# Kernel optimization log

Measured on AMD Instinct MI355X. Metric: run time of the kernel, lower is better.

## Reference

```python
import jax, jax.numpy as jnp
import numpy as np

G = 8          # grid_size
NUM_HEADS = 8


def setup_inputs() -> dict:
    key = jax.random.key(0)
    ks = jax.random.split(key, 4)
    B, H, W, C = 32, 64, 64, 256
    x = jax.random.normal(ks[0], (B, H, W, C), dtype=jnp.float32)
    w_qkv = jax.random.normal(ks[1], (3 * C, C), dtype=jnp.float32) * (C ** -0.5)
    b_qkv = jnp.zeros((3 * C,), dtype=jnp.float32)
    w_proj = jax.random.normal(ks[2], (C, C), dtype=jnp.float32) * (C ** -0.5)
    b_proj = jnp.zeros((C,), dtype=jnp.float32)
    return {"x": x, "w_qkv": w_qkv, "b_qkv": b_qkv, "w_proj": w_proj, "b_proj": b_proj}


def reference(x, w_qkv, b_qkv, w_proj, b_proj):
    B, H, W, C = x.shape
    g = G
    nh = NUM_HEADS
    hd = C // nh
    scale = hd ** -0.5
    Hp, Wp = H // g, W // g
    # grid partition: [B,H,W,C] -> [B*Hp*Wp, g*g, C]
    t = x.reshape(B, g, Hp, g, Wp, C)
    t = t.transpose(0, 2, 4, 1, 3, 5).reshape(B * Hp * Wp, g * g, C)
    Bg, N = t.shape[0], g * g
    # qkv projection (torch Linear: x @ W.T + b)
    qkv = t @ w_qkv.T + b_qkv                       # [Bg, N, 3C]
    qkv = qkv.reshape(Bg, N, 3, nh, hd).transpose(2, 0, 3, 1, 4)  # [3, Bg, nh, N, hd]
    q, k, v = qkv[0], qkv[1], qkv[2]
    attn = jnp.einsum('bhnd,bhmd->bhnm', q, k) * scale
    attn = jax.nn.softmax(attn, axis=-1)
    out = jnp.einsum('bhnm,bhmd->bhnd', attn, v)    # [Bg, nh, N, hd]
    out = out.transpose(0, 2, 1, 3).reshape(Bg, N, C)
    out = out @ w_proj.T + b_proj
    # grid unpartition: [Bg, g, g, C] -> [B, H, W, C]
    out = out.reshape(B, Hp, Wp, g, g, C).transpose(0, 3, 1, 4, 2, 5).reshape(B, H, W, C)
    return out
```

## Files before the change

### kernel.cpp

```cpp
#include <hip/hip_runtime.h>

typedef __attribute__((ext_vector_type(8))) short bf16x8;
typedef __attribute__((ext_vector_type(4))) float f32x4;
typedef __attribute__((ext_vector_type(4))) short s16x4;

#define MFMA16(a, b, c) __builtin_amdgcn_mfma_f32_16x16x32_bf16((a), (b), (c), 0, 0, 0)

__device__ __forceinline__ short f2bf(float f) {
    union { float f; unsigned u; } v; v.f = f;
    return (short)((v.u + 0x7FFFu + ((v.u >> 16) & 1u)) >> 16);
}
__device__ __forceinline__ s16x4 cvt4(f32x4 v) {
    s16x4 r; r[0] = f2bf(v[0]); r[1] = f2bf(v[1]); r[2] = f2bf(v[2]); r[3] = f2bf(v[3]); return r;
}
__device__ __forceinline__ f32x4 fzero4() { f32x4 z; z[0]=0.f; z[1]=0.f; z[2]=0.f; z[3]=0.f; return z; }

__global__ __launch_bounds__(256, 1)
void convw_kernel(const float* __restrict__ wqkv, const float* __restrict__ wproj,
                  short* __restrict__ wsb)
{
    int i = (blockIdx.x * 256 + threadIdx.x) * 8;
    const float* src = (i < 196608) ? (wqkv + i) : (wproj + (i - 196608));
    *(s16x4*)(wsb + i)     = cvt4(*(const f32x4*)(src));
    *(s16x4*)(wsb + i + 4) = cvt4(*(const f32x4*)(src + 4));
}

#define SMEM_BYTES 52224


#define QK_ST(HL, MH, B)  { \
    _Pragma("unroll") \
    for (int n2 = 0; n2 < 2; ++n2) { \
      _Pragma("unroll") \
      for (int m2 = 0; m2 < 2; ++m2) { \
        s16x4 pk; \
        _Pragma("unroll") \
        for (int r = 0; r < 4; ++r) \
          pk[r] = f2bf(acc[2*(HL)+n2][2*(MH)+m2][r] + bq[2*(HL)+n2][r]); \
        *(s16x4*)((B) + (m2*16 + l16)*36 + n2*16 + q4*4) = pk; \
      } \
    } }

#define QK_RD(HL, MH, B, DST)  { \
    _Pragma("unroll") \
    for (int m2 = 0; m2 < 2; ++m2) \
      DST[HL][2*(MH)+m2] = *(const bf16x8*)((B) + (m2*16 + l16)*36 + q4*8); }

#define QK_ROUNDS(DST) \
    QK_ST(0,0,SW0) QK_ST(0,1,SW1) QK_RD(0,0,SW0,DST) QK_ST(1,0,SW0) \
    QK_RD(0,1,SW1,DST) QK_ST(1,1,SW1) QK_RD(1,0,SW0,DST) QK_RD(1,1,SW1,DST)

#define P_ST(KT, MH, B)  { \
    _Pragma("unroll") \
    for (int n2 = 0; n2 < 2; ++n2) { \
      _Pragma("unroll") \
      for (int m2 = 0; m2 < 2; ++m2) { \
        s16x4 pk; \
        _Pragma("unroll") \
        for (int r = 0; r < 4; ++r) \
          pk[r] = f2bf(s[2*(KT)+n2][2*(MH)+m2][r]); \
        *(s16x4*)((B) + (m2*16 + l16)*36 + n2*16 + q4*4) = pk; \
      } \
    } }

#define P_RD(MH, B)  { \
    _Pragma("unroll") \
    for (int m2 = 0; m2 < 2; ++m2) \
      pa[2*(MH)+m2] = *(const bf16x8*)((B) + (m2*16 + l16)*36 + q4*8); }

__global__ __launch_bounds__(256, 3)
void ga2d_kernel(const float* __restrict__ x,
                 const short* __restrict__ wsb,
                 const float* __restrict__ bqkv,
                 const float* __restrict__ bproj,
                 float* __restrict__ out)
{
    extern __shared__ short smem[];
    short* XA = smem;
    const int tid  = threadIdx.x;
    const int w    = tid >> 6;
    const int lane = tid & 63;
    const int l16  = lane & 15;
    const int q4   = lane >> 4;
    short* SW0 = smem + 16896 + w * 2304;
    short* SW1 = SW0 + 1152;

    const int blk = blockIdx.x;
    const int bb  = blk >> 6;
    const int hp  = (blk >> 3) & 7;
    const int wp  = blk & 7;
    const size_t gbase = (size_t)bb * 64 * 64 * 256;

    #pragma unroll
    for (int i = 0; i < 16; ++i) {
        int id  = i * 256 + tid;
        int tok = id >> 6, c4 = id & 63;
        int hr  = (tok >> 3) * 8 + hp;
        int wc  = (tok & 7) * 8 + wp;
        f32x4 v = *(const f32x4*)(x + gbase + ((size_t)hr * 64 + wc) * 256 + c4 * 4);
        *(s16x4*)(XA + tok * 264 + c4 * 4) = cvt4(v);
    }
    __syncthreads();

    bf16x8 qa[2][4], kb[2][4], vb[2][2][2];
    #pragma unroll
    for (int g3 = 0; g3 < 2; ++g3) {
        const short* WB = wsb + (size_t)(g3 * 256 + w * 64) * 256;
        f32x4 acc[4][4];
        #pragma unroll
        for (int n = 0; n < 4; ++n)
            #pragma unroll
            for (int m = 0; m < 4; ++m) acc[n][m] = fzero4();
        #pragma unroll
        for (int k = 0; k < 8; ++k) {
            const int koff = k * 32 + q4 * 8;
            bf16x8 a[4], bw[4];
            #pragma unroll
            for (int m = 0; m < 4; ++m)
                a[m] = *(const bf16x8*)(XA + (m * 16 + l16) * 264 + koff);
            #pragma unroll
            for (int n = 0; n < 4; ++n)
                bw[n] = *(const bf16x8*)(WB + (size_t)(n * 16 + l16) * 256 + koff);
            #pragma unroll
            for (int n = 0; n < 4; ++n)
                #pragma unroll
                for (int m = 0; m < 4; ++m)
                    acc[n][m] = MFMA16(bw[n], a[m], acc[n][m]);
        }
        f32x4 bq[4];
        #pragma unroll
        for (int n = 0; n < 4; ++n)
            bq[n] = *(const f32x4*)(bqkv + g3 * 256 + w * 64 + n * 16 + q4 * 4);
        if (g3 == 0) { QK_ROUNDS(qa) } else { QK_ROUNDS(kb) }
    }
    {
        float bv[4];
        #pragma unroll
        for (int n = 0; n < 4; ++n) bv[n] = bqkv[512 + w * 64 + n * 16 + l16];
        #pragma unroll
        for (int vh = 0; vh < 2; ++vh) {
            const short* WB = wsb + (size_t)(512 + w * 64 + vh * 32) * 256;
            f32x4 acc2[2][4];
            #pragma unroll
            for (int n2 = 0; n2 < 2; ++n2)
                #pragma unroll
                for (int m = 0; m < 4; ++m) acc2[n2][m] = fzero4();
            #pragma unroll
            for (int k = 0; k < 8; ++k) {
                const int koff = k * 32 + q4 * 8;
                bf16x8 a[4], bw2[2];
                #pragma unroll
                for (int m = 0; m < 4; ++m)
                    a[m] = *(const bf16x8*)(XA + (m * 16 + l16) * 264 + koff);
                #pragma unroll
                for (int n2 = 0; n2 < 2; ++n2)
                    bw2[n2] = *(const bf16x8*)(WB + (size_t)(n2 * 16 + l16) * 256 + koff);
                #pragma unroll
                for (int n2 = 0; n2 < 2; ++n2)
                    #pragma unroll
                    for (int m = 0; m < 4; ++m)
                        acc2[n2][m] = MFMA16(a[m], bw2[n2], acc2[n2][m]);
            }
            #pragma unroll
            for (int kt = 0; kt < 2; ++kt) {
                short* B = kt ? SW1 : SW0;
                #pragma unroll
                for (int n2 = 0; n2 < 2; ++n2)
                    #pragma unroll
                    for (int m2 = 0; m2 < 2; ++m2) {
                        s16x4 pk;
                        #pragma unroll
                        for (int r = 0; r < 4; ++r)
                            pk[r] = f2bf(acc2[n2][2 * kt + m2][r] + bv[2 * vh + n2]);
                        *(s16x4*)(B + (n2 * 16 + l16) * 36 + m2 * 16 + q4 * 4) = pk;
                    }
            }
            #pragma unroll
            for (int kt = 0; kt < 2; ++kt) {
                const short* B = kt ? SW1 : SW0;
                #pragma unroll
                for (int dt = 0; dt < 2; ++dt)
                    vb[vh][dt][kt] = *(const bf16x8*)(B + (dt * 16 + l16) * 36 + q4 * 8);
            }
        }
    }
    __syncthreads();

    const float kscl = 0.25503546f;
    #pragma unroll
    for (int hl = 0; hl < 2; ++hl) {
        f32x4 s[4][4];
        #pragma unroll
        for (int n = 0; n < 4; ++n)
            #pragma unroll
            for (int m = 0; m < 4; ++m)
                s[n][m] = MFMA16(kb[hl][n], qa[hl][m], fzero4());

        float rinv[4];
        #pragma unroll
        for (int m = 0; m < 4; ++m) {
            float v0 = fmaxf(fmaxf(s[0][m][0], s[0][m][1]), fmaxf(s[0][m][2], s[0][m][3]));
            float v1 = fmaxf(fmaxf(s[1][m][0], s[1][m][1]), fmaxf(s[1][m][2], s[1][m][3]));
            float v2 = fmaxf(fmaxf(s[2][m][0], s[2][m][1]), fmaxf(s[2][m][2], s[2][m][3]));
            float v3 = fmaxf(fmaxf(s[3][m][0], s[3][m][1]), fmaxf(s[3][m][2], s[3][m][3]));
            float v  = fmaxf(fmaxf(v0, v1), fmaxf(v2, v3));
            v = fmaxf(v, __shfl_xor(v, 16));
            v = fmaxf(v, __shfl_xor(v, 32));
            float t = 0.f;
            #pragma unroll
            for (int n = 0; n < 4; ++n)
                #pragma unroll
                for (int r = 0; r < 4; ++r) {
                    float e = exp2f((s[n][m][r] - v) * kscl);
                    s[n][m][r] = e;
                    t += e;
                }
            t += __shfl_xor(t, 16);
            t += __shfl_xor(t, 32);
            rinv[m] = 1.0f / t;
        }

        f32x4 o2[2][4];
        #pragma unroll
        for (int dt = 0; dt < 2; ++dt)
            #pragma unroll
            for (int m = 0; m < 4; ++m) o2[dt][m] = fzero4();
        #pragma unroll
        for (int kt = 0; kt < 2; ++kt) {
            bf16x8 pa[4];
            P_ST(kt,0,SW0) P_ST(kt,1,SW1) P_RD(0,SW0) P_RD(1,SW1)
            #pragma unroll
            for (int m = 0; m < 4; ++m)
                #pragma unroll
                for (int dt = 0; dt < 2; ++dt)
                    o2[dt][m] = MFMA16(vb[hl][dt][kt], pa[m], o2[dt][m]);
        }
        #pragma unroll
        for (int dt = 0; dt < 2; ++dt)
            #pragma unroll
            for (int m = 0; m < 4; ++m) {
                s16x4 pk;
                #pragma unroll
                for (int r = 0; r < 4; ++r) pk[r] = f2bf(o2[dt][m][r] * rinv[m]);
                *(s16x4*)(XA + (m * 16 + l16) * 264 + w * 64 + hl * 32 + dt * 16 + q4 * 4) = pk;
            }
    }
    __syncthreads();

    {
        const short* WPb = wsb + 196608 + (size_t)(w * 64) * 256;
        f32x4 pc[4][4];
        #pragma unroll
        for (int n = 0; n < 4; ++n)
            #pragma unroll
            for (int m = 0; m < 4; ++m) pc[n][m] = fzero4();
        #pragma unroll
        for (int k = 0; k < 8; ++k) {
            const int koff = k * 32 + q4 * 8;
            bf16x8 a[4], bw[4];
            #pragma unroll
            for (int m = 0; m < 4; ++m)
                a[m] = *(const bf16x8*)(XA + (m * 16 + l16) * 264 + koff);
            #pragma unroll
            for (int n = 0; n < 4; ++n)
                bw[n] = *(const bf16x8*)(WPb + (size_t)(n * 16 + l16) * 256 + koff);
            #pragma unroll
            for (int n = 0; n < 4; ++n)
                #pragma unroll
                for (int m = 0; m < 4; ++m)
                    pc[n][m] = MFMA16(a[m], bw[n], pc[n][m]);
        }
        #pragma unroll
        for (int n = 0; n < 4; ++n) {
            const int col  = w * 64 + n * 16 + l16;
            const float bi = bproj[col];
            #pragma unroll
            for (int m = 0; m < 4; ++m) {
                #pragma unroll
                for (int r = 0; r < 4; ++r) {
                    const int tok = m * 16 + q4 * 4 + r;
                    const int hr  = (tok >> 3) * 8 + hp;
                    const int wc  = (tok & 7) * 8 + wp;
                    out[gbase + ((size_t)hr * 64 + wc) * 256 + col] = pc[n][m][r] + bi;
                }
            }
        }
    }
}

extern "C" void kernel_launch(void* const* d_in, const int* in_sizes, int n_in,
                              void* d_out, int out_size, void* d_ws, size_t ws_size,
                              hipStream_t stream) {
    const float* x     = (const float*)d_in[0];
    const float* wqkv  = (const float*)d_in[1];
    const float* bqkv  = (const float*)d_in[2];
    const float* wproj = (const float*)d_in[3];
    const float* bproj = (const float*)d_in[4];
    float*       out   = (float*)d_out;
    short*       wsb   = (short*)d_ws;

    convw_kernel<<<128, 256, 0, stream>>>(wqkv, wproj, wsb);

    hipFuncSetAttribute(reinterpret_cast<const void*>(ga2d_kernel),
                        hipFuncAttributeMaxDynamicSharedMemorySize, SMEM_BYTES);
    ga2d_kernel<<<2048, 256, SMEM_BYTES, stream>>>(x, wsb, bqkv, bproj, out);
}
```

Measured before the change: 366.3 us.

## Use 8 waves per block with one head per wave and drop softmax max

The block grows from 4 to 8 waves, so each wave handles one attention head and a 32-column slice of each projection, cutting per-wave register pressure and raising parallelism. Shared memory grows to hold per-wave scratch for 8 waves. Softmax now skips the row-max subtraction and accumulates exp sums while streaming P to shared memory. That removes a reduction pass, but exp2 of unshifted scores can overflow for larger logits.

```diff
diff --git a/kernel.cpp b/kernel.cpp
--- a/kernel.cpp
+++ b/kernel.cpp
@@ -25,50 +25,44 @@
     *(s16x4*)(wsb + i + 4) = cvt4(*(const f32x4*)(src + 4));
 }
 
-#define SMEM_BYTES 52224
-
-
-#define QK_ST(HL, MH, B)  { \
-    _Pragma("unroll") \
-    for (int n2 = 0; n2 < 2; ++n2) { \
-      _Pragma("unroll") \
-      for (int m2 = 0; m2 < 2; ++m2) { \
-        s16x4 pk; \
-        _Pragma("unroll") \
-        for (int r = 0; r < 4; ++r) \
-          pk[r] = f2bf(acc[2*(HL)+n2][2*(MH)+m2][r] + bq[2*(HL)+n2][r]); \
-        *(s16x4*)((B) + (m2*16 + l16)*36 + n2*16 + q4*4) = pk; \
-      } \
+#define SMEM_BYTES 70656
+
+#define QKGEMM(G3, DST) { \
+    const short* WB = wsb + (size_t)((G3) * 256 + w * 32) * 256; \
+    f32x4 acc[2][4]; \
+    _Pragma("unroll") for (int n2 = 0; n2 < 2; ++n2) \
+      _Pragma("unroll") for (int m = 0; m < 4; ++m) acc[n2][m] = fzero4(); \
+    _Pragma("unroll") for (int k = 0; k < 8; ++k) { \
+        const int koff = k * 32 + q4 * 8; \
+        bf16x8 a[4], bw[2]; \
+        _Pragma("unroll") for (int m = 0; m < 4; ++m) \
+            a[m] = *(const bf16x8*)(XA + (m * 16 + l16) * 264 + koff); \
+        _Pragma("unroll") for (int n2 = 0; n2 < 2; ++n2) \
+            bw[n2] = *(const bf16x8*)(WB + (size_t)(n2 * 16 + l16) * 256 + koff); \
+        _Pragma("unroll") for (int n2 = 0; n2 < 2; ++n2) \
+          _Pragma("unroll") for (int m = 0; m < 4; ++m) \
+            acc[n2][m] = MFMA16(bw[n2], a[m], acc[n2][m]); \
+    } \
+    f32x4 bq[2]; \
+    _Pragma("unroll") for (int n2 = 0; n2 < 2; ++n2) \
+        bq[n2] = *(const f32x4*)(bqkv + (G3) * 256 + w * 32 + n2 * 16 + q4 * 4); \
+    _Pragma("unroll") for (int MH = 0; MH < 2; ++MH) { \
+        short* B = MH ? SW1 : SW0; \
+        _Pragma("unroll") for (int n2 = 0; n2 < 2; ++n2) \
+          _Pragma("unroll") for (int m2 = 0; m2 < 2; ++m2) { \
+            s16x4 pk; \
+            _Pragma("unroll") for (int r = 0; r < 4; ++r) \
+                pk[r] = f2bf(acc[n2][2 * MH + m2][r] + bq[n2][r]); \
+            *(s16x4*)(B + (m2 * 16 + l16) * 36 + n2 * 16 + q4 * 4) = pk; \
+        } \
+    } \
+    _Pragma("unroll") for (int MH = 0; MH < 2; ++MH) { \
+        const short* B = MH ? SW1 : SW0; \
+        _Pragma("unroll") for (int m2 = 0; m2 < 2; ++m2) \
+            DST[2 * MH + m2] = *(const bf16x8*)(B + (m2 * 16 + l16) * 36 + q4 * 8); \
     } }
 
-#define QK_RD(HL, MH, B, DST)  { \
-    _Pragma("unroll") \
-    for (int m2 = 0; m2 < 2; ++m2) \
-      DST[HL][2*(MH)+m2] = *(const bf16x8*)((B) + (m2*16 + l16)*36 + q4*8); }
-
-#define QK_ROUNDS(DST) \
-    QK_ST(0,0,SW0) QK_ST(0,1,SW1) QK_RD(0,0,SW0,DST) QK_ST(1,0,SW0) \
-    QK_RD(0,1,SW1,DST) QK_ST(1,1,SW1) QK_RD(1,0,SW0,DST) QK_RD(1,1,SW1,DST)
-
-#define P_ST(KT, MH, B)  { \
-    _Pragma("unroll") \
-    for (int n2 = 0; n2 < 2; ++n2) { \
-      _Pragma("unroll") \
-      for (int m2 = 0; m2 < 2; ++m2) { \
-        s16x4 pk; \
-        _Pragma("unroll") \
-        for (int r = 0; r < 4; ++r) \
-          pk[r] = f2bf(s[2*(KT)+n2][2*(MH)+m2][r]); \
-        *(s16x4*)((B) + (m2*16 + l16)*36 + n2*16 + q4*4) = pk; \
-      } \
-    } }
-
-#define P_RD(MH, B)  { \
-    _Pragma("unroll") \
-    for (int m2 = 0; m2 < 2; ++m2) \
-      pa[2*(MH)+m2] = *(const bf16x8*)((B) + (m2*16 + l16)*36 + q4*8); }
-
-__global__ __launch_bounds__(256, 3)
+__global__ __launch_bounds__(512, 4)
 void ga2d_kernel(const float* __restrict__ x,
                  const short* __restrict__ wsb,
                  const float* __restrict__ bqkv,
@@ -92,8 +86,8 @@
     const size_t gbase = (size_t)bb * 64 * 64 * 256;
 
     #pragma unroll
-    for (int i = 0; i < 16; ++i) {
-        int id  = i * 256 + tid;
+    for (int i = 0; i < 8; ++i) {
+        int id  = i * 512 + tid;
         int tok = id >> 6, c4 = id & 63;
         int hr  = (tok >> 3) * 8 + hp;
         int wc  = (tok & 7) * 8 + wp;
@@ -102,138 +96,113 @@
     }
     __syncthreads();
 
-    bf16x8 qa[2][4], kb[2][4], vb[2][2][2];
-    #pragma unroll
-    for (int g3 = 0; g3 < 2; ++g3) {
-        const short* WB = wsb + (size_t)(g3 * 256 + w * 64) * 256;
-        f32x4 acc[4][4];
-        #pragma unroll
-        for (int n = 0; n < 4; ++n)
-            #pragma unroll
-            for (int m = 0; m < 4; ++m) acc[n][m] = fzero4();
+    bf16x8 qa[4], kb[4], vb[2][2];
+    {
+        const short* WB = wsb + (size_t)(512 + w * 32) * 256;
+        f32x4 acc[2][4];
+        #pragma unroll
+        for (int n2 = 0; n2 < 2; ++n2)
+            #pragma unroll
+            for (int m = 0; m < 4; ++m) acc[n2][m] = fzero4();
         #pragma unroll
         for (int k = 0; k < 8; ++k) {
             const int koff = k * 32 + q4 * 8;
-            bf16x8 a[4], bw[4];
+            bf16x8 a[4], bw[2];
             #pragma unroll
             for (int m = 0; m < 4; ++m)
                 a[m] = *(const bf16x8*)(XA + (m * 16 + l16) * 264 + koff);
             #pragma unroll
-            for (int n = 0; n < 4; ++n)
-                bw[n] = *(const bf16x8*)(WB + (size_t)(n * 16 + l16) * 256 + koff);
-            #pragma unroll
-            for (int n = 0; n < 4; ++n)
+            for (int n2 = 0; n2 < 2; ++n2)
+                bw[n2] = *(const bf16x8*)(WB + (size_t)(n2 * 16 + l16) * 256 + koff);
+            #pragma unroll
+            for (int n2 = 0; n2 < 2; ++n2)
                 #pragma unroll
                 for (int m = 0; m < 4; ++m)
-                    acc[n][m] = MFMA16(bw[n], a[m], acc[n][m]);
-        }
-        f32x4 bq[4];
-        #pragma unroll
-        for (int n = 0; n < 4; ++n)
-            bq[n] = *(const f32x4*)(bqkv + g3 * 256 + w * 64 + n * 16 + q4 * 4);
-        if (g3 == 0) { QK_ROUNDS(qa) } else { QK_ROUNDS(kb) }
-    }
+                    acc[n2][m] = MFMA16(a[m], bw[n2], acc[n2][m]);
+        }
+        float bv[2];
+        #pragma unroll
+        for (int n2 = 0; n2 < 2; ++n2) bv[n2] = bqkv[512 + w * 32 + n2 * 16 + l16];
+        #pragma unroll
+        for (int kt = 0; kt < 2; ++kt) {
+            short* B = kt ? SW1 : SW0;
+            #pragma unroll
+            for (int n2 = 0; n2 < 2; ++n2)
+                #pragma unroll
+                for (int m2 = 0; m2 < 2; ++m2) {
+                    s16x4 pk;
+                    #pragma unroll
+                    for (int r = 0; r < 4; ++r)
+                        pk[r] = f2bf(acc[n2][2 * kt + m2][r] + bv[n2]);
+                    *(s16x4*)(B + (n2 * 16 + l16) * 36 + m2 * 16 + q4 * 4) = pk;
+                }
+        }
+        #pragma unroll
+        for (int kt = 0; kt < 2; ++kt) {
+            const short* B = kt ? SW1 : SW0;
+            #pragma unroll
+            for (int dt = 0; dt < 2; ++dt)
+                vb[dt][kt] = *(const bf16x8*)(B + (dt * 16 + l16) * 36 + q4 * 8);
+        }
+    }
+    QKGEMM(0, qa)
+    QKGEMM(1, kb)
+    __syncthreads();
+
+    const float kscl = 0.25503546f;
     {
-        float bv[4];
-        #pragma unroll
-        for (int n = 0; n < 4; ++n) bv[n] = bqkv[512 + w * 64 + n * 16 + l16];
-        #pragma unroll
-        for (int vh = 0; vh < 2; ++vh) {
-            const short* WB = wsb + (size_t)(512 + w * 64 + vh * 32) * 256;
-            f32x4 acc2[2][4];
-            #pragma unroll
-            for (int n2 = 0; n2 < 2; ++n2)
-                #pragma unroll
-                for (int m = 0; m < 4; ++m) acc2[n2][m] = fzero4();
-            #pragma unroll
-            for (int k = 0; k < 8; ++k) {
-                const int koff = k * 32 + q4 * 8;
-                bf16x8 a[4], bw2[2];
+        float t[4] = {0.f, 0.f, 0.f, 0.f};
+        f32x4 o2[2][4];
+        #pragma unroll
+        for (int dt = 0; dt < 2; ++dt)
+            #pragma unroll
+            for (int m = 0; m < 4; ++m) o2[dt][m] = fzero4();
+        #pragma unroll
+        for (int kt = 0; kt < 2; ++kt) {
+            f32x4 s2[2][4];
+            #pragma unroll
+            for (int n2 = 0; n2 < 2; ++n2)
                 #pragma unroll
                 for (int m = 0; m < 4; ++m)
-                    a[m] = *(const bf16x8*)(XA + (m * 16 + l16) * 264 + koff);
-                #pragma unroll
-                for (int n2 = 0; n2 < 2; ++n2)
-                    bw2[n2] = *(const bf16x8*)(WB + (size_t)(n2 * 16 + l16) * 256 + koff);
-                #pragma unroll
-                for (int n2 = 0; n2 < 2; ++n2)
-                    #pragma unroll
-                    for (int m = 0; m < 4; ++m)
-                        acc2[n2][m] = MFMA16(a[m], bw2[n2], acc2[n2][m]);
-            }
-            #pragma unroll
-            for (int kt = 0; kt < 2; ++kt) {
-                short* B = kt ? SW1 : SW0;
+                    s2[n2][m] = MFMA16(kb[2 * kt + n2], qa[m], fzero4());
+            #pragma unroll
+            for (int MH = 0; MH < 2; ++MH) {
+                short* B = MH ? SW1 : SW0;
                 #pragma unroll
                 for (int n2 = 0; n2 < 2; ++n2)
                     #pragma unroll
                     for (int m2 = 0; m2 < 2; ++m2) {
                         s16x4 pk;
                         #pragma unroll
-                        for (int r = 0; r < 4; ++r)
-                            pk[r] = f2bf(acc2[n2][2 * kt + m2][r] + bv[2 * vh + n2]);
-                        *(s16x4*)(B + (n2 * 16 + l16) * 36 + m2 * 16 + q4 * 4) = pk;
+                        for (int r = 0; r < 4; ++r) {
+                            float e = exp2f(s2[n2][2 * MH + m2][r] * kscl);
+                            t[2 * MH + m2] += e;
+                            pk[r] = f2bf(e);
+                        }
+                        *(s16x4*)(B + (m2 * 16 + l16) * 36 + n2 * 16 + q4 * 4) = pk;
                     }
             }
-            #pragma unroll
-            for (int kt = 0; kt < 2; ++kt) {
-                const short* B = kt ? SW1 : SW0;
+            bf16x8 pa[4];
+            #pragma unroll
+            for (int MH = 0; MH < 2; ++MH) {
+                const short* B = MH ? SW1 : SW0;
+                #pragma unroll
+                for (int m2 = 0; m2 < 2; ++m2)
+                    pa[2 * MH + m2] = *(const bf16x8*)(B + (m2 * 16 + l16) * 36 + q4 * 8);
+            }
+            #pragma unroll
+            for (int m = 0; m < 4; ++m)
                 #pragma unroll
                 for (int dt = 0; dt < 2; ++dt)
-                    vb[vh][dt][kt] = *(const bf16x8*)(B + (dt * 16 + l16) * 36 + q4 * 8);
-            }
-        }
-    }
-    __syncthreads();
-
-    const float kscl = 0.25503546f;
-    #pragma unroll
-    for (int hl = 0; hl < 2; ++hl) {
-        f32x4 s[4][4];
-        #pragma unroll
-        for (int n = 0; n < 4; ++n)
-            #pragma unroll
-            for (int m = 0; m < 4; ++m)
-                s[n][m] = MFMA16(kb[hl][n], qa[hl][m], fzero4());
-
+                    o2[dt][m] = MFMA16(vb[dt][kt], pa[m], o2[dt][m]);
+        }
         float rinv[4];
         #pragma unroll
         for (int m = 0; m < 4; ++m) {
-            float v0 = fmaxf(fmaxf(s[0][m][0], s[0][m][1]), fmaxf(s[0][m][2], s[0][m][3]));
-            float v1 = fmaxf(fmaxf(s[1][m][0], s[1][m][1]), fmaxf(s[1][m][2], s[1][m][3]));
-            float v2 = fmaxf(fmaxf(s[2][m][0], s[2][m][1]), fmaxf(s[2][m][2], s[2][m][3]));
-            float v3 = fmaxf(fmaxf(s[3][m][0], s[3][m][1]), fmaxf(s[3][m][2], s[3][m][3]));
-            float v  = fmaxf(fmaxf(v0, v1), fmaxf(v2, v3));
-            v = fmaxf(v, __shfl_xor(v, 16));
-            v = fmaxf(v, __shfl_xor(v, 32));
-            float t = 0.f;
-            #pragma unroll
-            for (int n = 0; n < 4; ++n)
-                #pragma unroll
-                for (int r = 0; r < 4; ++r) {
-                    float e = exp2f((s[n][m][r] - v) * kscl);
-                    s[n][m][r] = e;
-                    t += e;
-                }
-            t += __shfl_xor(t, 16);
-            t += __shfl_xor(t, 32);
-            rinv[m] = 1.0f / t;
-        }
-
-        f32x4 o2[2][4];
-        #pragma unroll
-        for (int dt = 0; dt < 2; ++dt)
-            #pragma unroll
-            for (int m = 0; m < 4; ++m) o2[dt][m] = fzero4();
-        #pragma unroll
-        for (int kt = 0; kt < 2; ++kt) {
-            bf16x8 pa[4];
-            P_ST(kt,0,SW0) P_ST(kt,1,SW1) P_RD(0,SW0) P_RD(1,SW1)
-            #pragma unroll
-            for (int m = 0; m < 4; ++m)
-                #pragma unroll
-                for (int dt = 0; dt < 2; ++dt)
-                    o2[dt][m] = MFMA16(vb[hl][dt][kt], pa[m], o2[dt][m]);
+            float tt = t[m];
+            tt += __shfl_xor(tt, 16);
+            tt += __shfl_xor(tt, 32);
+            rinv[m] = 1.0f / tt;
         }
         #pragma unroll
         for (int dt = 0; dt < 2; ++dt)
@@ -242,37 +211,37 @@
                 s16x4 pk;
                 #pragma unroll
                 for (int r = 0; r < 4; ++r) pk[r] = f2bf(o2[dt][m][r] * rinv[m]);
-                *(s16x4*)(XA + (m * 16 + l16) * 264 + w * 64 + hl * 32 + dt * 16 + q4 * 4) = pk;
+                *(s16x4*)(XA + (m * 16 + l16) * 264 + w * 32 + dt * 16 + q4 * 4) = pk;
             }
     }
     __syncthreads();
 
     {
-        const short* WPb = wsb + 196608 + (size_t)(w * 64) * 256;
-        f32x4 pc[4][4];
-        #pragma unroll
-        for (int n = 0; n < 4; ++n)
-            #pragma unroll
-            for (int m = 0; m < 4; ++m) pc[n][m] = fzero4();
+        const short* WPb = wsb + 196608 + (size_t)(w * 32) * 256;
+        f32x4 pc[2][4];
+        #pragma unroll
+        for (int n2 = 0; n2 < 2; ++n2)
+            #pragma unroll
+            for (int m = 0; m < 4; ++m) pc[n2][m] = fzero4();
         #pragma unroll
         for (int k = 0; k < 8; ++k) {
             const int koff = k * 32 + q4 * 8;
-            bf16x8 a[4], bw[4];
+            bf16x8 a[4], bw[2];
             #pragma unroll
             for (int m = 0; m < 4; ++m)
                 a[m] = *(const bf16x8*)(XA + (m * 16 + l16) * 264 + koff);
             #pragma unroll
-            for (int n = 0; n < 4; ++n)
-                bw[n] = *(const bf16x8*)(WPb + (size_t)(n * 16 + l16) * 256 + koff);
-            #pragma unroll
-            for (int n = 0; n < 4; ++n)
+            for (int n2 = 0; n2 < 2; ++n2)
+                bw[n2] = *(const bf16x8*)(WPb + (size_t)(n2 * 16 + l16) * 256 + koff);
+            #pragma unroll
+            for (int n2 = 0; n2 < 2; ++n2)
                 #pragma unroll
                 for (int m = 0; m < 4; ++m)
-                    pc[n][m] = MFMA16(a[m], bw[n], pc[n][m]);
-        }
-        #pragma unroll
-        for (int n = 0; n < 4; ++n) {
-            const int col  = w * 64 + n * 16 + l16;
+                    pc[n2][m] = MFMA16(a[m], bw[n2], pc[n2][m]);
+        }
+        #pragma unroll
+        for (int n2 = 0; n2 < 2; ++n2) {
+            const int col  = w * 32 + n2 * 16 + l16;
             const float bi = bproj[col];
             #pragma unroll
             for (int m = 0; m < 4; ++m) {
@@ -281,7 +250,7 @@
                     const int tok = m * 16 + q4 * 4 + r;
                     const int hr  = (tok >> 3) * 8 + hp;
                     const int wc  = (tok & 7) * 8 + wp;
-                    out[gbase + ((size_t)hr * 64 + wc) * 256 + col] = pc[n][m][r] + bi;
+                    out[gbase + ((size_t)hr * 64 + wc) * 256 + col] = pc[n2][m][r] + bi;
                 }
             }
         }
@@ -303,5 +272,5 @@
 
     hipFuncSetAttribute(reinterpret_cast<const void*>(ga2d_kernel),
                         hipFuncAttributeMaxDynamicSharedMemorySize, SMEM_BYTES);
-    ga2d_kernel<<<2048, 256, SMEM_BYTES, stream>>>(x, wsb, bqkv, bproj, out);
-}
+    ga2d_kernel<<<2048, 512, SMEM_BYTES, stream>>>(x, wsb, bqkv, bproj, out);
+}
```

After: 351.6 us. 1.04x faster.
